# Performance work log

Measured on AMD Instinct MI355X. Metric: run time of the kernel, lower is better.

Reference implementation:

```python
import jax, jax.numpy as jnp
import numpy as np

B, L, D = 2, 1536, 1024
H, P = 16, 1024
HD = P // H  # 64
K_SIZE = 5
DIFF_STEPS = 3
ALPHA = 0.02
NEG = -1e9
EPS = 1e-9


def setup_inputs() -> dict:
    key = jax.random.key(0)
    ks = jax.random.split(key, 12)
    s = 0.02
    hidden_states = jax.random.normal(ks[0], (B, L, D), dtype=jnp.float32)
    attention_mask = jax.random.randint(ks[1], (B, L), 0, 2, dtype=jnp.int32)
    Wq = jax.random.normal(ks[2], (D, P), dtype=jnp.float32) * s
    bq = jax.random.normal(ks[3], (P,), dtype=jnp.float32) * s
    Wk = jax.random.normal(ks[4], (D, P), dtype=jnp.float32) * s
    bk = jax.random.normal(ks[5], (P,), dtype=jnp.float32) * s
    Wv = jax.random.normal(ks[6], (D, P), dtype=jnp.float32) * s
    bv = jax.random.normal(ks[7], (P,), dtype=jnp.float32) * s
    Wo = jax.random.normal(ks[8], (P, D), dtype=jnp.float32) * s
    bo = jax.random.normal(ks[9], (D,), dtype=jnp.float32) * s
    kernel_w = jax.random.normal(ks[10], (K_SIZE,), dtype=jnp.float32)
    return {"hidden_states": hidden_states, "attention_mask": attention_mask,
            "Wq": Wq, "bq": bq, "Wk": Wk, "bk": bk, "Wv": Wv, "bv": bv,
            "Wo": Wo, "bo": bo, "kernel_w": kernel_w}


def _causal_smooth(p, w):
    # p: (B,H,Lq,Lk); causal cross-correlation matching F.conv1d(pad=k-1)[:Lk]
    k = w.shape[0]
    Lk = p.shape[-1]
    pp = jnp.pad(p, ((0, 0), (0, 0), (0, 0), (k - 1, 0)))
    out = w[0] * pp[..., 0:Lk]
    for j in range(1, k):
        out = out + w[j] * pp[..., j:j + Lk]
    return out


def reference(hidden_states, attention_mask, Wq, bq, Wk, bk, Wv, bv, Wo, bo, kernel_w):
    mask_f = attention_mask.astype(hidden_states.dtype)  # (B,Lk), 1=keep
    additive = (1.0 - mask_f) * NEG                       # (B,Lk)
    key_valid = (attention_mask > 0).astype(hidden_states.dtype)

    Q = (hidden_states @ Wq + bq).reshape(B, L, H, HD)
    Kt = (hidden_states @ Wk + bk).reshape(B, L, H, HD)
    V = (hidden_states @ Wv + bv).reshape(B, L, H, HD)

    scores = jnp.einsum('bqhd,bkhd->bhqk', Q, Kt) / np.sqrt(HD).astype(np.float32)
    scores = scores + additive[:, None, None, :]
    p = jax.nn.softmax(scores, axis=-1)  # (B,H,Lq,Lk)

    w = jax.nn.softmax(kernel_w)  # (k,)
    kv4 = key_valid[:, None, None, :]
    for _ in range(DIFF_STEPS):
        ps = _causal_smooth(p, w)
        ps = ps * kv4
        ps = ps / (jnp.sum(ps, axis=-1, keepdims=True) + EPS)
        p = (1.0 - ALPHA) * p + ALPHA * ps

    attn = jnp.einsum('bhqk,bkhd->bqhd', p, V).reshape(B, L, P)
    return attn @ Wo + bo
```

## Files before the change

kernel.cpp:

```cpp
#include <hip/hip_runtime.h>

#define BB 2
#define LL 1536
#define DD 1024
#define HH 16
#define HDD 64
#define PP 1024
#define PBS 1544

typedef __attribute__((ext_vector_type(8))) __bf16 bf16x8;
typedef __attribute__((ext_vector_type(4))) float f32x4;
typedef __attribute__((ext_vector_type(2))) float f32x2;

__device__ __forceinline__ float b2f(unsigned short u) {
  unsigned int x = ((unsigned int)u) << 16;
  return __builtin_bit_cast(float, x);
}
__device__ __forceinline__ unsigned short f2b(float f) {
  unsigned int x = __builtin_bit_cast(unsigned int, f);
  unsigned int r = (x + 0x7FFFu + ((x >> 16) & 1u)) >> 16;
  return (unsigned short)r;
}
__device__ __forceinline__ bf16x8 ldb8(const unsigned short* p) {
  return __builtin_bit_cast(bf16x8, *(const uint4*)p);
}
__device__ __forceinline__ f32x2 mk2(float a, float b) {
  f32x2 r;
  r.x = a;
  r.y = b;
  return r;
}
__device__ __forceinline__ void gl_lds16(const unsigned short* g,
                                         unsigned short* l) {
  __builtin_amdgcn_global_load_lds(
      (const __attribute__((address_space(1))) void*)g,
      (__attribute__((address_space(3))) void*)l, 16, 0, 0);
}

__global__ __launch_bounds__(256) void cast_hs(const float* __restrict__ src,
                                               unsigned short* __restrict__ dst) {
  const int idx = (blockIdx.x * 256 + threadIdx.x) * 8;
  float4 a = *(const float4*)(src + idx);
  float4 b = *(const float4*)(src + idx + 4);
  uint4 u;
  u.x = (unsigned int)f2b(a.x) | ((unsigned int)f2b(a.y) << 16);
  u.y = (unsigned int)f2b(a.z) | ((unsigned int)f2b(a.w) << 16);
  u.z = (unsigned int)f2b(b.x) | ((unsigned int)f2b(b.y) << 16);
  u.w = (unsigned int)f2b(b.z) | ((unsigned int)f2b(b.w) << 16);
  *(uint4*)(dst + idx) = u;
}

__global__ __launch_bounds__(256) void transpose_w(
    const float* __restrict__ Wq, const float* __restrict__ Wk,
    const float* __restrict__ Wv, const float* __restrict__ Wo,
    unsigned short* __restrict__ WT) {
  __shared__ float tile[64][68];
  const float* W = (blockIdx.z == 0) ? Wq
                   : (blockIdx.z == 1) ? Wk
                   : (blockIdx.z == 2) ? Wv : Wo;
  unsigned short* O = WT + (size_t)blockIdx.z * 1024 * 1024;
  const int t = threadIdx.x;
  const int r0 = blockIdx.y * 64;
  const int c0 = blockIdx.x * 64;
#pragma unroll
  for (int i = 0; i < 4; ++i) {
    const int row = (t >> 4) + i * 16;
    const int col = (t & 15) * 4;
    *(float4*)&tile[row][col] = *(const float4*)&W[(size_t)(r0 + row) * 1024 + c0 + col];
  }
  __syncthreads();
#pragma unroll
  for (int i = 0; i < 4; ++i) {
    const int n = (t >> 4) + i * 16;
    const int k4 = (t & 15) * 4;
    uint2 u;
    u.x = (unsigned int)f2b(tile[k4 + 0][n]) |
          ((unsigned int)f2b(tile[k4 + 1][n]) << 16);
    u.y = (unsigned int)f2b(tile[k4 + 2][n]) |
          ((unsigned int)f2b(tile[k4 + 3][n]) << 16);
    *(uint2*)&O[(size_t)(c0 + n) * 1024 + r0 + k4] = u;
  }
}

template <int MODE>
__device__ __forceinline__ void gemm_mfma_body(
    const unsigned short* __restrict__ A, const unsigned short* __restrict__ Bt,
    const float* __restrict__ bias, void* __restrict__ Cout) {
  __shared__ unsigned short As[64 * 32];
  __shared__ unsigned short Bs[128 * 32];
  const int t = threadIdx.x;
  const int lane = t & 63;
  const int w = t >> 6;
  const int quad = lane >> 4;
  const int lc = lane & 15;
  const int m0 = blockIdx.y * 64, n0 = blockIdx.x * 128;

  const int sr = lane >> 2;
  const int sk = (lane & 3) * 8;
  const unsigned short* gA = A + (size_t)(m0 + w * 16 + sr) * 1024 + sk;
  const unsigned short* gB0 = Bt + (size_t)(n0 + w * 32 + sr) * 1024 + sk;
  const unsigned short* gB1 = gB0 + 16 * 1024;
  unsigned short* lA = As + w * 512;
  unsigned short* lB0 = Bs + w * 1024;
  unsigned short* lB1 = Bs + w * 1024 + 512;

  const int mrow0 = (w & 1) * 32, ncol0 = (w >> 1) * 64;

  f32x4 acc[2][4];
#pragma unroll
  for (int i = 0; i < 2; ++i)
#pragma unroll
    for (int j = 0; j < 4; ++j) acc[i][j] = (f32x4){0.f, 0.f, 0.f, 0.f};

  for (int k0 = 0; k0 < 1024; k0 += 32) {
    __syncthreads();
    gl_lds16(gA + k0, lA);
    gl_lds16(gB0 + k0, lB0);
    gl_lds16(gB1 + k0, lB1);
    __syncthreads();
    bf16x8 af[2], bfr[4];
#pragma unroll
    for (int i = 0; i < 2; ++i)
      af[i] = ldb8(&As[(mrow0 + i * 16 + lc) * 32 + quad * 8]);
#pragma unroll
    for (int j = 0; j < 4; ++j)
      bfr[j] = ldb8(&Bs[(ncol0 + j * 16 + lc) * 32 + quad * 8]);
#pragma unroll
    for (int i = 0; i < 2; ++i)
#pragma unroll
      for (int j = 0; j < 4; ++j)
        acc[i][j] =
            __builtin_amdgcn_mfma_f32_16x16x32_bf16(af[i], bfr[j], acc[i][j], 0, 0, 0);
  }

#pragma unroll
  for (int i = 0; i < 2; ++i) {
    const int row0 = m0 + mrow0 + i * 16 + quad * 4;
#pragma unroll
    for (int jj = 0; jj < 4; ++jj) {
      const int col = n0 + ncol0 + jj * 16 + lc;
      const float bz = bias[col];
      float o[4];
#pragma unroll
      for (int r = 0; r < 4; ++r) o[r] = acc[i][jj][r] + bz;
      if constexpr (MODE == 0) {
#pragma unroll
        for (int r = 0; r < 4; ++r)
          ((unsigned short*)Cout)[(size_t)(row0 + r) * 1024 + col] =
              f2b(o[r] * 0.125f);
      } else if constexpr (MODE == 1) {
        const int bb = row0 / LL;
        const int kl = row0 - bb * LL;
        const int ktl = kl >> 4;
        const int m = kl & 15;
        const int hh = col >> 6;
        const int hd = col & 63;
        const int f = hd >> 5;
        const int qk = (hd >> 3) & 3;
        const int j = hd & 7;
        unsigned short* KF = (unsigned short*)Cout;
        const size_t base =
            (((size_t)(bb * HH + hh) * 96 + ktl) * 2 + f) * 512 +
            (qk * 16 + m) * 8 + j;
#pragma unroll
        for (int r = 0; r < 4; ++r) KF[base + r * 8] = f2b(o[r]);
      } else if constexpr (MODE == 2) {
        const int bb = row0 / LL;
        const int kl = row0 - bb * LL;
        const int hh = col >> 6;
        const int hd = col & 63;
        const int hg = hd >> 4;
        const int lcv = hd & 15;
        const int tile = (kl >> 5);
        const int qv = (kl >> 3) & 3;
        const int j0 = kl & 7;
        unsigned short* VF = (unsigned short*)Cout;
        const size_t base =
            (((size_t)(bb * HH + hh) * 4 + hg) * 48 + tile) * 512 +
            (qv * 16 + lcv) * 8 + j0;
        uint2 u;
        u.x = (unsigned int)f2b(o[0]) | ((unsigned int)f2b(o[1]) << 16);
        u.y = (unsigned int)f2b(o[2]) | ((unsigned int)f2b(o[3]) << 16);
        *(uint2*)&VF[base] = u;
      } else {
#pragma unroll
        for (int r = 0; r < 4; ++r)
          ((float*)Cout)[(size_t)(row0 + r) * 1024 + col] = o[r];
      }
    }
  }
}

__global__ __launch_bounds__(256) void qkv_gemm(
    const unsigned short* __restrict__ hsb, const unsigned short* __restrict__ WT,
    const float* __restrict__ bq, const float* __restrict__ bk,
    const float* __restrict__ bv, unsigned short* __restrict__ Qb,
    unsigned short* __restrict__ KF, unsigned short* __restrict__ VF) {
  if (blockIdx.z == 0) {
    gemm_mfma_body<0>(hsb, WT, bq, Qb);
  } else if (blockIdx.z == 1) {
    gemm_mfma_body<1>(hsb, WT + 1024 * 1024, bk, KF);
  } else {
    gemm_mfma_body<2>(hsb, WT + 2 * 1024 * 1024, bv, VF);
  }
}

__global__ __launch_bounds__(256) void out_gemm(
    const unsigned short* __restrict__ ctxb,
    const unsigned short* __restrict__ WoT, const float* __restrict__ bo,
    float* __restrict__ out) {
  gemm_mfma_body<3>(ctxb, WoT, bo, out);
}

__global__ __launch_bounds__(512, 4) void attn_kernel(
    const unsigned short* __restrict__ Qb, const unsigned short* __restrict__ KF,
    const unsigned short* __restrict__ VF, const int* __restrict__ mask,
    const float* __restrict__ kernel_w, unsigned short* __restrict__ ctxb) {
  __shared__ __align__(16) unsigned short p_b[16][PBS];
  __shared__ unsigned int kvb[50];
  __shared__ float red_s[8][16];

  const int t = threadIdx.x;
  const int lane = t & 63;
  const int w = t >> 6;
  const int quad = lane >> 4;
  const int lc = lane & 15;
  const int b = blockIdx.z, h = blockIdx.y;
  const int q0 = blockIdx.x * 16;

  if (t < 2) kvb[48 + t] = 0;
#pragma unroll
  for (int r = 0; r < 3; ++r) {
    const int idx = r * 512 + t;
    unsigned long long bal = __ballot(mask[b * LL + idx] > 0);
    if (lane == 0) {
      const int base = (r * 512 + w * 64) >> 5;
      kvb[base] = (unsigned int)bal;
      kvb[base + 1] = (unsigned int)(bal >> 32);
    }
  }
  __syncthreads();

  const unsigned short* qp = Qb + ((size_t)(b * LL + q0 + lc)) * PP + h * HDD;
  const bf16x8 qb0 = ldb8(qp + quad * 8);
  const bf16x8 qb1 = ldb8(qp + 32 + quad * 8);
  float sc[12][4];
  const unsigned short* kfb =
      KF + (((size_t)(b * HH + h) * 96 + w) * 2) * 512 + lane * 8;
#pragma unroll
  for (int j = 0; j < 12; ++j) {
    bf16x8 ka0 = ldb8(kfb + j * 8192);
    bf16x8 ka1 = ldb8(kfb + j * 8192 + 512);
    f32x4 acc = {0.f, 0.f, 0.f, 0.f};
    acc = __builtin_amdgcn_mfma_f32_16x16x32_bf16(ka0, qb0, acc, 0, 0, 0);
    acc = __builtin_amdgcn_mfma_f32_16x16x32_bf16(ka1, qb1, acc, 0, 0, 0);
    sc[j][0] = acc[0];
    sc[j][1] = acc[1];
    sc[j][2] = acc[2];
    sc[j][3] = acc[3];
  }

  const int kbase = w * 16 + quad * 4;
  const int gamma = kbase >> 5;
  const int beta = kbase & 31;
  float s = 0.f;
#pragma unroll
  for (int j = 0; j < 12; ++j) {
    const unsigned int w4 = (kvb[j * 4 + gamma] >> beta) & 0xFu;
#pragma unroll
    for (int r = 0; r < 4; ++r) {
      float e = ((w4 >> r) & 1u) ? __expf(sc[j][r]) : 0.f;
      sc[j][r] = e;
      s += e;
    }
  }
  s += __shfl_xor(s, 16, 64);
  s += __shfl_xor(s, 32, 64);
  if (lane < 16) red_s[w][lane] = s;
  __syncthreads();
  float tot = 0.f;
#pragma unroll
  for (int ww = 0; ww < 8; ++ww) tot += red_s[ww][lc];
  const float inv = 1.f / tot;
#pragma unroll
  for (int j = 0; j < 12; ++j) {
    uint2 u;
    u.x = (unsigned int)f2b(sc[j][0] * inv) |
          ((unsigned int)f2b(sc[j][1] * inv) << 16);
    u.y = (unsigned int)f2b(sc[j][2] * inv) |
          ((unsigned int)f2b(sc[j][3] * inv) << 16);
    *(uint2*)&p_b[lc][j * 128 + kbase] = u;
  }
  __syncthreads();

  float wr[5];
  {
    float k0 = kernel_w[0], k1 = kernel_w[1], k2 = kernel_w[2],
          k3 = kernel_w[3], k4 = kernel_w[4];
    float km = fmaxf(fmaxf(fmaxf(k0, k1), fmaxf(k2, k3)), k4);
    float e0 = __expf(k0 - km), e1 = __expf(k1 - km), e2 = __expf(k2 - km),
          e3 = __expf(k3 - km), e4 = __expf(k4 - km);
    float es = e0 + e1 + e2 + e3 + e4;
    wr[0] = e4 / es;
    wr[1] = e3 / es;
    wr[2] = e2 / es;
    wr[3] = e1 / es;
    wr[4] = e0 / es;
  }
  unsigned int db;
  {
    const int w0i = (lane * 24) >> 5, sh = (lane * 24) & 31;
    unsigned long long kw2 =
        ((unsigned long long)kvb[w0i + 1] << 32) | (unsigned long long)kvb[w0i];
    db = (unsigned int)((kw2 >> sh) & 0xFFFFFFu);
  }
  f32x2 fm2[12];
#pragma unroll
  for (int i = 0; i < 12; ++i)
    fm2[i] = mk2((float)((db >> (2 * i)) & 1u), (float)((db >> (2 * i + 1)) & 1u));

  for (int rr = 0; rr < 2; ++rr) {
    const int row = w * 2 + rr;
    f32x2 pg[12];
#pragma unroll
    for (int c = 0; c < 3; ++c) {
      uint4 v = *(const uint4*)&p_b[row][lane * 24 + c * 8];
      unsigned int ws4[4] = {v.x, v.y, v.z, v.w};
#pragma unroll
      for (int q = 0; q < 4; ++q)
        pg[c * 4 + q] =
            mk2(__builtin_bit_cast(float, ws4[q] << 16),
                __builtin_bit_cast(float, ws4[q] & 0xFFFF0000u));
    }
#pragma unroll
    for (int step = 0; step < 3; ++step) {
      float h1 = __shfl_up(pg[11].y, 1);
      float h2 = __shfl_up(pg[11].x, 1);
      float h3 = __shfl_up(pg[10].y, 1);
      float h4 = __shfl_up(pg[10].x, 1);
      if (lane == 0) h1 = h2 = h3 = h4 = 0.f;
      f32x2 ps2[12];
      ps2[0] = wr[0] * pg[0] + wr[1] * mk2(h1, pg[0].x) + wr[2] * mk2(h2, h1) +
               wr[3] * mk2(h3, h2) + wr[4] * mk2(h4, h3);
      ps2[1] = wr[0] * pg[1] + wr[1] * mk2(pg[0].y, pg[1].x) + wr[2] * pg[0] +
               wr[3] * mk2(h1, pg[0].x) + wr[4] * mk2(h2, h1);
#pragma unroll
      for (int i = 2; i < 12; ++i)
        ps2[i] = wr[0] * pg[i] + wr[1] * mk2(pg[i - 1].y, pg[i].x) +
                 wr[2] * pg[i - 1] + wr[3] * mk2(pg[i - 2].y, pg[i - 1].x) +
                 wr[4] * pg[i - 2];
      f32x2 acc2 = mk2(0.f, 0.f);
#pragma unroll
      for (int i = 0; i < 12; ++i) {
        ps2[i] *= fm2[i];
        acc2 += ps2[i];
      }
      float sv = acc2.x + acc2.y;
#pragma unroll
      for (int off = 1; off < 64; off <<= 1) sv += __shfl_xor(sv, off, 64);
      const float pinv = 0.02f / (sv + 1e-9f);
#pragma unroll
      for (int i = 0; i < 12; ++i) pg[i] = 0.98f * pg[i] + ps2[i] * pinv;
    }
#pragma unroll
    for (int c = 0; c < 3; ++c) {
      unsigned int uw[4];
#pragma unroll
      for (int q = 0; q < 4; ++q)
        uw[q] = (unsigned int)f2b(pg[c * 4 + q].x) |
                ((unsigned int)f2b(pg[c * 4 + q].y) << 16);
      uint4 u;
      u.x = uw[0];
      u.y = uw[1];
      u.z = uw[2];
      u.w = uw[3];
      *(uint4*)&p_b[row][lane * 24 + c * 8] = u;
    }
  }
  __syncthreads();

  const int cidx = (w & 3) * 16 + lc;
  const int gbase = (w >> 2) * 12;
  const unsigned short* vfb =
      VF + ((((size_t)(b * HH + h) * 4 + (w & 3)) * 48 + (w >> 2) * 24) * 512) +
      lane * 8;
  f32x4 oacc = {0.f, 0.f, 0.f, 0.f};
#pragma unroll
  for (int g = 0; g < 12; ++g) {
    const int gg = gbase + g;
#pragma unroll
    for (int c = 0; c < 2; ++c) {
      bf16x8 pa = ldb8(&p_b[lc][gg * 64 + c * 32 + quad * 8]);
      bf16x8 vf = ldb8(vfb + (g * 2 + c) * 512);
      oacc = __builtin_amdgcn_mfma_f32_16x16x32_bf16(pa, vf, oacc, 0, 0, 0);
    }
  }
  __syncthreads();
  float* pscr = (float*)&p_b[0][0];
  if (w >= 4) {
    const int idx = ((((w - 4) * 4 + quad) * 16) + lc) * 4;
    *(float4*)(pscr + idx) =
        make_float4(oacc[0], oacc[1], oacc[2], oacc[3]);
  }
  __syncthreads();
  if (w < 4) {
    const int idx = (((w * 4 + quad) * 16) + lc) * 4;
    float4 pr = *(const float4*)(pscr + idx);
    float o[4] = {oacc[0] + pr.x, oacc[1] + pr.y, oacc[2] + pr.z,
                  oacc[3] + pr.w};
#pragma unroll
    for (int r = 0; r < 4; ++r)
      ctxb[((size_t)(b * LL + q0 + quad * 4 + r)) * PP + h * HDD + cidx] =
          f2b(o[r]);
  }
}

extern "C" void kernel_launch(void* const* d_in, const int* in_sizes, int n_in,
                              void* d_out, int out_size, void* d_ws,
                              size_t ws_size, hipStream_t stream) {
  const float* hs = (const float*)d_in[0];
  const int* mask = (const int*)d_in[1];
  const float* Wq = (const float*)d_in[2];
  const float* bq = (const float*)d_in[3];
  const float* Wk = (const float*)d_in[4];
  const float* bk = (const float*)d_in[5];
  const float* Wv = (const float*)d_in[6];
  const float* bv = (const float*)d_in[7];
  const float* Wo = (const float*)d_in[8];
  const float* bo = (const float*)d_in[9];
  const float* kw = (const float*)d_in[10];

  const size_t NBLP = (size_t)BB * LL * PP;
  unsigned short* Qb = (unsigned short*)d_ws;
  unsigned short* KF = Qb + NBLP;
  unsigned short* VF = KF + NBLP;
  unsigned short* ctxb = VF + NBLP;
  unsigned short* hsb = ctxb + NBLP;
  unsigned short* WT = hsb + NBLP;

  dim3 blk(256);
  cast_hs<<<dim3(1536), blk, 0, stream>>>(hs, hsb);
  transpose_w<<<dim3(16, 16, 4), blk, 0, stream>>>(Wq, Wk, Wv, Wo, WT);
  qkv_gemm<<<dim3(8, 48, 3), blk, 0, stream>>>(hsb, WT, bq, bk, bv, Qb, KF, VF);
  attn_kernel<<<dim3(96, 16, 2), dim3(512), 0, stream>>>(Qb, KF, VF, mask, kw,
                                                         ctxb);
  out_gemm<<<dim3(8, 48, 1), blk, 0, stream>>>(ctxb, WT + 3 * 1024 * 1024, bo,
                                               (float*)d_out);
}
```

Before: 251.1 us.

## Fuse prep kernels, enlarge GEMM tiles to 128x128, pre-swizzle Q, use DPP wave reduction

```diff
diff --git a/kernel.cpp b/kernel.cpp
--- a/kernel.cpp
+++ b/kernel.cpp
@@ -37,48 +37,68 @@
       (__attribute__((address_space(3))) void*)l, 16, 0, 0);
 }
 
-__global__ __launch_bounds__(256) void cast_hs(const float* __restrict__ src,
-                                               unsigned short* __restrict__ dst) {
-  const int idx = (blockIdx.x * 256 + threadIdx.x) * 8;
-  float4 a = *(const float4*)(src + idx);
-  float4 b = *(const float4*)(src + idx + 4);
-  uint4 u;
-  u.x = (unsigned int)f2b(a.x) | ((unsigned int)f2b(a.y) << 16);
-  u.y = (unsigned int)f2b(a.z) | ((unsigned int)f2b(a.w) << 16);
-  u.z = (unsigned int)f2b(b.x) | ((unsigned int)f2b(b.y) << 16);
-  u.w = (unsigned int)f2b(b.z) | ((unsigned int)f2b(b.w) << 16);
-  *(uint4*)(dst + idx) = u;
-}
-
-__global__ __launch_bounds__(256) void transpose_w(
+template <int CTRL>
+__device__ __forceinline__ float dppadd(float x) {
+  int s = __builtin_amdgcn_update_dpp(0, __builtin_bit_cast(int, x), CTRL, 0xf,
+                                      0xf, true);
+  return x + __builtin_bit_cast(float, s);
+}
+__device__ __forceinline__ float wave_sum64(float x) {
+  x = dppadd<0x111>(x);
+  x = dppadd<0x112>(x);
+  x = dppadd<0x114>(x);
+  x = dppadd<0x118>(x);
+  x = dppadd<0x142>(x);
+  x = dppadd<0x143>(x);
+  return __builtin_bit_cast(
+      float, __builtin_amdgcn_readlane(__builtin_bit_cast(int, x), 63));
+}
+
+__global__ __launch_bounds__(256) void prep(
+    const float* __restrict__ hs, unsigned short* __restrict__ hsb,
     const float* __restrict__ Wq, const float* __restrict__ Wk,
     const float* __restrict__ Wv, const float* __restrict__ Wo,
     unsigned short* __restrict__ WT) {
-  __shared__ float tile[64][68];
-  const float* W = (blockIdx.z == 0) ? Wq
-                   : (blockIdx.z == 1) ? Wk
-                   : (blockIdx.z == 2) ? Wv : Wo;
-  unsigned short* O = WT + (size_t)blockIdx.z * 1024 * 1024;
+  const int bid = blockIdx.x;
   const int t = threadIdx.x;
-  const int r0 = blockIdx.y * 64;
-  const int c0 = blockIdx.x * 64;
-#pragma unroll
-  for (int i = 0; i < 4; ++i) {
-    const int row = (t >> 4) + i * 16;
-    const int col = (t & 15) * 4;
-    *(float4*)&tile[row][col] = *(const float4*)&W[(size_t)(r0 + row) * 1024 + c0 + col];
-  }
-  __syncthreads();
-#pragma unroll
-  for (int i = 0; i < 4; ++i) {
-    const int n = (t >> 4) + i * 16;
-    const int k4 = (t & 15) * 4;
-    uint2 u;
-    u.x = (unsigned int)f2b(tile[k4 + 0][n]) |
-          ((unsigned int)f2b(tile[k4 + 1][n]) << 16);
-    u.y = (unsigned int)f2b(tile[k4 + 2][n]) |
-          ((unsigned int)f2b(tile[k4 + 3][n]) << 16);
-    *(uint2*)&O[(size_t)(c0 + n) * 1024 + r0 + k4] = u;
+  if (bid < 1536) {
+    const int idx = bid * 2048 + t * 8;
+    float4 a = *(const float4*)(hs + idx);
+    float4 b = *(const float4*)(hs + idx + 4);
+    uint4 u;
+    u.x = (unsigned int)f2b(a.x) | ((unsigned int)f2b(a.y) << 16);
+    u.y = (unsigned int)f2b(a.z) | ((unsigned int)f2b(a.w) << 16);
+    u.z = (unsigned int)f2b(b.x) | ((unsigned int)f2b(b.y) << 16);
+    u.w = (unsigned int)f2b(b.z) | ((unsigned int)f2b(b.w) << 16);
+    *(uint4*)(hsb + idx) = u;
+  } else {
+    __shared__ float tile[64][68];
+    const int t2 = bid - 1536;
+    const int z = t2 >> 8;
+    const int bx = t2 & 15, by = (t2 >> 4) & 15;
+    const float* W = (z == 0) ? Wq : (z == 1) ? Wk : (z == 2) ? Wv : Wo;
+    unsigned short* O = WT + (size_t)z * 1024 * 1024;
+    const int r0 = by * 64;
+    const int c0 = bx * 64;
+#pragma unroll
+    for (int i = 0; i < 4; ++i) {
+      const int row = (t >> 4) + i * 16;
+      const int col = (t & 15) * 4;
+      *(float4*)&tile[row][col] =
+          *(const float4*)&W[(size_t)(r0 + row) * 1024 + c0 + col];
+    }
+    __syncthreads();
+#pragma unroll
+    for (int i = 0; i < 4; ++i) {
+      const int n = (t >> 4) + i * 16;
+      const int k4 = (t & 15) * 4;
+      uint2 u;
+      u.x = (unsigned int)f2b(tile[k4 + 0][n]) |
+            ((unsigned int)f2b(tile[k4 + 1][n]) << 16);
+      u.y = (unsigned int)f2b(tile[k4 + 2][n]) |
+            ((unsigned int)f2b(tile[k4 + 3][n]) << 16);
+      *(uint2*)&O[(size_t)(c0 + n) * 1024 + r0 + k4] = u;
+    }
   }
 }
 
@@ -86,47 +106,50 @@
 __device__ __forceinline__ void gemm_mfma_body(
     const unsigned short* __restrict__ A, const unsigned short* __restrict__ Bt,
     const float* __restrict__ bias, void* __restrict__ Cout) {
-  __shared__ unsigned short As[64 * 32];
+  __shared__ unsigned short As[128 * 32];
   __shared__ unsigned short Bs[128 * 32];
   const int t = threadIdx.x;
   const int lane = t & 63;
   const int w = t >> 6;
   const int quad = lane >> 4;
   const int lc = lane & 15;
-  const int m0 = blockIdx.y * 64, n0 = blockIdx.x * 128;
+  const int m0 = blockIdx.y * 128, n0 = blockIdx.x * 128;
 
   const int sr = lane >> 2;
   const int sk = (lane & 3) * 8;
-  const unsigned short* gA = A + (size_t)(m0 + w * 16 + sr) * 1024 + sk;
-  const unsigned short* gB0 = Bt + (size_t)(n0 + w * 32 + sr) * 1024 + sk;
-  const unsigned short* gB1 = gB0 + 16 * 1024;
-  unsigned short* lA = As + w * 512;
-  unsigned short* lB0 = Bs + w * 1024;
-  unsigned short* lB1 = Bs + w * 1024 + 512;
-
-  const int mrow0 = (w & 1) * 32, ncol0 = (w >> 1) * 64;
-
-  f32x4 acc[2][4];
-#pragma unroll
-  for (int i = 0; i < 2; ++i)
+  const unsigned short* ga0 = A + (size_t)(m0 + w * 32 + sr) * 1024 + sk;
+  const unsigned short* ga1 = ga0 + 16 * 1024;
+  const unsigned short* gb0 = Bt + (size_t)(n0 + w * 32 + sr) * 1024 + sk;
+  const unsigned short* gb1 = gb0 + 16 * 1024;
+  unsigned short* la0 = As + w * 1024;
+  unsigned short* la1 = As + w * 1024 + 512;
+  unsigned short* lb0 = Bs + w * 1024;
+  unsigned short* lb1 = Bs + w * 1024 + 512;
+
+  const int mrow0 = (w >> 1) * 64, ncol0 = (w & 1) * 64;
+
+  f32x4 acc[4][4];
+#pragma unroll
+  for (int i = 0; i < 4; ++i)
 #pragma unroll
     for (int j = 0; j < 4; ++j) acc[i][j] = (f32x4){0.f, 0.f, 0.f, 0.f};
 
   for (int k0 = 0; k0 < 1024; k0 += 32) {
     __syncthreads();
-    gl_lds16(gA + k0, lA);
-    gl_lds16(gB0 + k0, lB0);
-    gl_lds16(gB1 + k0, lB1);
+    gl_lds16(ga0 + k0, la0);
+    gl_lds16(ga1 + k0, la1);
+    gl_lds16(gb0 + k0, lb0);
+    gl_lds16(gb1 + k0, lb1);
     __syncthreads();
-    bf16x8 af[2], bfr[4];
-#pragma unroll
-    for (int i = 0; i < 2; ++i)
+    bf16x8 af[4], bfr[4];
+#pragma unroll
+    for (int i = 0; i < 4; ++i)
       af[i] = ldb8(&As[(mrow0 + i * 16 + lc) * 32 + quad * 8]);
 #pragma unroll
     for (int j = 0; j < 4; ++j)
       bfr[j] = ldb8(&Bs[(ncol0 + j * 16 + lc) * 32 + quad * 8]);
 #pragma unroll
-    for (int i = 0; i < 2; ++i)
+    for (int i = 0; i < 4; ++i)
 #pragma unroll
       for (int j = 0; j < 4; ++j)
         acc[i][j] =
@@ -134,7 +157,7 @@
   }
 
 #pragma unroll
-  for (int i = 0; i < 2; ++i) {
+  for (int i = 0; i < 4; ++i) {
     const int row0 = m0 + mrow0 + i * 16 + quad * 4;
 #pragma unroll
     for (int jj = 0; jj < 4; ++jj) {
@@ -144,10 +167,21 @@
 #pragma unroll
       for (int r = 0; r < 4; ++r) o[r] = acc[i][jj][r] + bz;
       if constexpr (MODE == 0) {
-#pragma unroll
-        for (int r = 0; r < 4; ++r)
-          ((unsigned short*)Cout)[(size_t)(row0 + r) * 1024 + col] =
-              f2b(o[r] * 0.125f);
+        const int bb = row0 / LL;
+        const int ql = row0 - bb * LL;
+        const int qt = ql >> 4;
+        const int m = ql & 15;
+        const int hh = col >> 6;
+        const int hd = col & 63;
+        const int f = hd >> 5;
+        const int qk = (hd >> 3) & 3;
+        const int j = hd & 7;
+        unsigned short* QF = (unsigned short*)Cout;
+        const size_t base =
+            (((size_t)(bb * HH + hh) * 96 + qt) * 2 + f) * 512 +
+            (qk * 16 + m) * 8 + j;
+#pragma unroll
+        for (int r = 0; r < 4; ++r) QF[base + r * 8] = f2b(o[r] * 0.125f);
       } else if constexpr (MODE == 1) {
         const int bb = row0 / LL;
         const int kl = row0 - bb * LL;
@@ -194,10 +228,10 @@
 __global__ __launch_bounds__(256) void qkv_gemm(
     const unsigned short* __restrict__ hsb, const unsigned short* __restrict__ WT,
     const float* __restrict__ bq, const float* __restrict__ bk,
-    const float* __restrict__ bv, unsigned short* __restrict__ Qb,
+    const float* __restrict__ bv, unsigned short* __restrict__ QF,
     unsigned short* __restrict__ KF, unsigned short* __restrict__ VF) {
   if (blockIdx.z == 0) {
-    gemm_mfma_body<0>(hsb, WT, bq, Qb);
+    gemm_mfma_body<0>(hsb, WT, bq, QF);
   } else if (blockIdx.z == 1) {
     gemm_mfma_body<1>(hsb, WT + 1024 * 1024, bk, KF);
   } else {
@@ -213,7 +247,7 @@
 }
 
 __global__ __launch_bounds__(512, 4) void attn_kernel(
-    const unsigned short* __restrict__ Qb, const unsigned short* __restrict__ KF,
+    const unsigned short* __restrict__ QF, const unsigned short* __restrict__ KF,
     const unsigned short* __restrict__ VF, const int* __restrict__ mask,
     const float* __restrict__ kernel_w, unsigned short* __restrict__ ctxb) {
   __shared__ __align__(16) unsigned short p_b[16][PBS];
@@ -241,9 +275,10 @@
   }
   __syncthreads();
 
-  const unsigned short* qp = Qb + ((size_t)(b * LL + q0 + lc)) * PP + h * HDD;
-  const bf16x8 qb0 = ldb8(qp + quad * 8);
-  const bf16x8 qb1 = ldb8(qp + 32 + quad * 8);
+  const unsigned short* qfb =
+      QF + (((size_t)(b * HH + h) * 96 + (q0 >> 4)) * 2) * 512 + lane * 8;
+  const bf16x8 qb0 = ldb8(qfb);
+  const bf16x8 qb1 = ldb8(qfb + 512);
   float sc[12][4];
   const unsigned short* kfb =
       KF + (((size_t)(b * HH + h) * 96 + w) * 2) * 512 + lane * 8;
@@ -278,10 +313,10 @@
   s += __shfl_xor(s, 32, 64);
   if (lane < 16) red_s[w][lane] = s;
   __syncthreads();
-  float tot = 0.f;
-#pragma unroll
-  for (int ww = 0; ww < 8; ++ww) tot += red_s[ww][lc];
-  const float inv = 1.f / tot;
+  float tot0 = 0.f;
+#pragma unroll
+  for (int ww = 0; ww < 8; ++ww) tot0 += red_s[ww][lc];
+  const float inv = 1.f / tot0;
 #pragma unroll
   for (int j = 0; j < 12; ++j) {
     uint2 u;
@@ -355,10 +390,8 @@
         ps2[i] *= fm2[i];
         acc2 += ps2[i];
       }
-      float sv = acc2.x + acc2.y;
-#pragma unroll
-      for (int off = 1; off < 64; off <<= 1) sv += __shfl_xor(sv, off, 64);
-      const float pinv = 0.02f / (sv + 1e-9f);
+      const float tot = wave_sum64(acc2.x + acc2.y);
+      const float pinv = 0.02f / (tot + 1e-9f);
 #pragma unroll
       for (int i = 0; i < 12; ++i) pg[i] = 0.98f * pg[i] + ps2[i] * pinv;
     }
@@ -431,19 +464,18 @@
   const float* kw = (const float*)d_in[10];
 
   const size_t NBLP = (size_t)BB * LL * PP;
-  unsigned short* Qb = (unsigned short*)d_ws;
-  unsigned short* KF = Qb + NBLP;
+  unsigned short* QF = (unsigned short*)d_ws;
+  unsigned short* KF = QF + NBLP;
   unsigned short* VF = KF + NBLP;
   unsigned short* ctxb = VF + NBLP;
   unsigned short* hsb = ctxb + NBLP;
   unsigned short* WT = hsb + NBLP;
 
   dim3 blk(256);
-  cast_hs<<<dim3(1536), blk, 0, stream>>>(hs, hsb);
-  transpose_w<<<dim3(16, 16, 4), blk, 0, stream>>>(Wq, Wk, Wv, Wo, WT);
-  qkv_gemm<<<dim3(8, 48, 3), blk, 0, stream>>>(hsb, WT, bq, bk, bv, Qb, KF, VF);
-  attn_kernel<<<dim3(96, 16, 2), dim3(512), 0, stream>>>(Qb, KF, VF, mask, kw,
+  prep<<<dim3(2560), blk, 0, stream>>>(hs, hsb, Wq, Wk, Wv, Wo, WT);
+  qkv_gemm<<<dim3(8, 24, 3), blk, 0, stream>>>(hsb, WT, bq, bk, bv, QF, KF, VF);
+  attn_kernel<<<dim3(96, 16, 2), dim3(512), 0, stream>>>(QF, KF, VF, mask, kw,
                                                          ctxb);
-  out_gemm<<<dim3(8, 48, 1), blk, 0, stream>>>(ctxb, WT + 3 * 1024 * 1024, bo,
+  out_gemm<<<dim3(8, 24, 1), blk, 0, stream>>>(ctxb, WT + 3 * 1024 * 1024, bo,
                                                (float*)d_out);
 }
```

Measured after the change: 242.6 us. 1.03x faster.
